# Kernel tuning notes

Hardware: AMD Instinct MI355X
Metric: run time of the kernel (lower is better)

Reference implementation:

```python
import jax, jax.numpy as jnp
import numpy as np

B, N, DIM = 4, 2048, 512
HEADS, DIM_HEAD = 8, 64
HIDDEN = HEADS * DIM_HEAD  # == DIM


def _rotary(t):
    # t: [b, h, n, d]; interleaved rotary (rotary-embedding-torch style), theta=10000
    n, d = t.shape[-2], t.shape[-1]
    inv_freq = 1.0 / (10000.0 ** (jnp.arange(0, d, 2, dtype=jnp.float32) / d))  # [d/2]
    freqs = jnp.arange(n, dtype=jnp.float32)[:, None] * inv_freq[None, :]        # [n, d/2]
    freqs = jnp.repeat(freqs, 2, axis=-1)                                        # [n, d]
    cos, sin = jnp.cos(freqs), jnp.sin(freqs)
    x1, x2 = t[..., ::2], t[..., 1::2]
    rot = jnp.stack((-x2, x1), axis=-1).reshape(t.shape)  # rotate_half, interleaved
    return t * cos + rot * sin


def setup_inputs() -> dict:
    key = jax.random.key(0)
    k1, k2, k3, k4 = jax.random.split(key, 4)
    x = jax.random.normal(k1, (B, N, DIM), dtype=jnp.float32)
    pos_bias = jax.random.normal(k2, (HEADS, N, N), dtype=jnp.float32)
    W_qkv = jax.random.normal(k3, (DIM, 3 * HIDDEN), dtype=jnp.float32) * (DIM ** -0.5)
    W_out = jax.random.normal(k4, (HIDDEN, DIM), dtype=jnp.float32) * (HIDDEN ** -0.5)
    return {"x": x, "pos_bias": pos_bias, "W_qkv": W_qkv, "W_out": W_out}


def reference(x, pos_bias, W_qkv, W_out):
    b, n, _ = x.shape
    qkv = x @ W_qkv                                   # [b, n, 3*h*d]
    q, k, v = jnp.split(qkv, 3, axis=-1)

    def to_heads(t):
        return t.reshape(b, n, HEADS, DIM_HEAD).transpose(0, 2, 1, 3)  # [b,h,n,d]

    q = to_heads(q) * (DIM_HEAD ** -0.5)
    k = to_heads(k)
    v = to_heads(v)
    q = _rotary(q)
    k = _rotary(k)
    sim = jnp.einsum('bhid,bhjd->bhij', q, k) + pos_bias[None]  # [b,h,n,n]
    attn = jax.nn.softmax(sim, axis=-1)                          # stable softmax (== amax-subtract + softmax)
    out = jnp.einsum('bhij,bhjd->bhid', attn, v)
    out = out.transpose(0, 2, 1, 3).reshape(b, n, HIDDEN)
    return out @ W_out
```

## Files before the change

kernel.cpp:

```cpp
#include <hip/hip_runtime.h>
#include <hip/hip_bf16.h>

#define DEV static __device__ __forceinline__

typedef __attribute__((ext_vector_type(8))) short s16x8;
typedef __attribute__((ext_vector_type(16))) float f32x16;

DEV float bf2f(short s) {
    unsigned u = ((unsigned)(unsigned short)s) << 16;
    union { unsigned u; float f; } c; c.u = u; return c.f;
}
DEV short f2bf(float f) {
    union { float f; unsigned u; } c; c.f = f;
    unsigned u = c.u;
    unsigned r = (u + 0x7FFFu + ((u >> 16) & 1u)) >> 16;
    return (short)r;
}

DEV f32x16 mfma(s16x8 a, s16x8 b, f32x16 c) {
    return __builtin_amdgcn_mfma_f32_32x32x16_bf16(a, b, c, 0, 0, 0);
}

__global__ void cvt_f32_bf16(const float* __restrict__ src,
                             short* __restrict__ dst, int n) {
    int i = (blockIdx.x * blockDim.x + threadIdx.x) * 4;
    if (i >= n) return;
    float4 v = *(const float4*)(src + i);
    short4 o;
    o.x = f2bf(v.x); o.y = f2bf(v.y); o.z = f2bf(v.z); o.w = f2bf(v.w);
    *(short4*)(dst + i) = o;
}

__global__ void rotab(float2* __restrict__ tab) {
    int idx = blockIdx.x * 256 + threadIdx.x;
    int n = idx >> 5, f = idx & 31;
    float inv = expf(-0.2878231366f * (float)f);
    float a = (float)n * inv;
    tab[idx] = make_float2(cosf(a), sinf(a));
}

__global__ void ktransf(const float* __restrict__ src, short* __restrict__ dst,
                        int R, int C) {
    __shared__ __align__(16) short t[32][33];
    int tx = threadIdx.x & 31, ty = threadIdx.x >> 5;
    int r0 = blockIdx.y * 32, c0 = blockIdx.x * 32;
    for (int i = 0; i < 32; i += 8)
        t[ty + i][tx] = f2bf(src[(size_t)(r0 + ty + i) * C + c0 + tx]);
    __syncthreads();
    for (int i = 0; i < 32; i += 8)
        dst[(size_t)(c0 + ty + i) * R + r0 + tx] = t[tx][ty + i];
}

__global__ __launch_bounds__(256) void gemm_qkv(
    const short* __restrict__ X, const short* __restrict__ WT,
    const float2* __restrict__ rtab,
    short* __restrict__ qws, short* __restrict__ kws, short* __restrict__ vt) {
    int wave = threadIdx.x >> 6, lane = threadIdx.x & 63;
    int l31 = lane & 31, lh = lane >> 5;
    int mw = blockIdx.x * 128 + (wave >> 1) * 64;
    int nw = blockIdx.y * 128 + (wave & 1) * 64;
    f32x16 acc[2][2] = {};
    const short* ap = X + (size_t)(mw + l31) * 512 + lh * 8;
    const short* bp = WT + (size_t)(nw + l31) * 512 + lh * 8;
#pragma unroll 4
    for (int k = 0; k < 512; k += 16) {
        s16x8 a0 = *(const s16x8*)(ap + k);
        s16x8 a1 = *(const s16x8*)(ap + 32 * 512 + k);
        s16x8 b0 = *(const s16x8*)(bp + k);
        s16x8 b1 = *(const s16x8*)(bp + 32 * 512 + k);
        acc[0][0] = mfma(a0, b0, acc[0][0]);
        acc[0][1] = mfma(a0, b1, acc[0][1]);
        acc[1][0] = mfma(a1, b0, acc[1][0]);
        acc[1][1] = mfma(a1, b1, acc[1][1]);
    }
#pragma unroll
    for (int ib = 0; ib < 2; ib++)
#pragma unroll
        for (int jb = 0; jb < 2; jb++) {
            int col = nw + jb * 32 + l31;
            int t = col >> 9;
            int cid = col & 511;
            int h = cid >> 6, d = cid & 63;
#pragma unroll
            for (int r = 0; r < 16; r++) {
                int row = (r & 3) + 8 * (r >> 2) + 4 * lh;
                int gm = mw + ib * 32 + row;
                int b = gm >> 11, n = gm & 2047;
                float v = acc[ib][jb][r];
                if (t == 0) v *= 0.125f;
                if (t < 2) {
                    float pv = __shfl_xor(v, 1);
                    float2 cs = rtab[n * 32 + (d >> 1)];
                    float o = (d & 1) ? (v * cs.x + pv * cs.y)
                                      : (v * cs.x - pv * cs.y);
                    short* dst = (t == 0) ? qws : kws;
                    dst[((size_t)(b * 8 + h) * 2048 + n) * 64 + d] = f2bf(o);
                } else {
                    vt[((size_t)(b * 8 + h) * 64 + d) * 2048 + n] = f2bf(v);
                }
            }
        }
}

#define PROW 72
__global__ __launch_bounds__(256) void attn(
    const short* __restrict__ qws, const short* __restrict__ kws,
    const short* __restrict__ vt, const float* __restrict__ bias,
    short* __restrict__ ows) {
    __shared__ __align__(16) short pls[4][32 * PROW];
    int wave = threadIdx.x >> 6, lane = threadIdx.x & 63;
    int l31 = lane & 31, lh = lane >> 5;
    int bh = blockIdx.y;
    int b = bh >> 3, h = bh & 7;
    int q0 = blockIdx.x * 128 + wave * 32;

    const short* qp = qws + ((size_t)bh * 2048 + q0 + l31) * 64 + lh * 8;
    s16x8 qf[4];
#pragma unroll
    for (int c = 0; c < 4; c++) qf[c] = *(const s16x8*)(qp + c * 16);

    f32x16 oa[2] = {};
    float lsum[16];
#pragma unroll
    for (int r = 0; r < 16; r++) lsum[r] = 0.f;
    short* pw = &pls[wave][0];
    const float* bias_base = bias + ((size_t)h * 2048 + q0) * 2048;

    for (int kt = 0; kt < 32; kt++) {
        int kb = kt * 64;
        const short* kp = kws + ((size_t)bh * 2048 + kb + l31) * 64 + lh * 8;
        f32x16 s0 = {}, s1 = {};
#pragma unroll
        for (int c = 0; c < 4; c++) {
            s16x8 k0 = *(const s16x8*)(kp + c * 16);
            s16x8 k1 = *(const s16x8*)(kp + 32 * 64 + c * 16);
            s0 = mfma(qf[c], k0, s0);
            s1 = mfma(qf[c], k1, s1);
        }
#pragma unroll
        for (int r = 0; r < 16; r++) {
            int row = (r & 3) + 8 * (r >> 2) + 4 * lh;
            const float* bp = bias_base + (size_t)row * 2048 + kb;
            float e0 = __expf(s0[r] + bp[l31]);
            float e1 = __expf(s1[r] + bp[32 + l31]);
            lsum[r] += e0 + e1;
            pw[row * PROW + l31] = f2bf(e0);
            pw[row * PROW + 32 + l31] = f2bf(e1);
        }
        const short* vp = vt + ((size_t)bh * 64 + l31) * 2048 + kb + lh * 8;
#pragma unroll
        for (int c = 0; c < 4; c++) {
            s16x8 pf = *(const s16x8*)(pw + l31 * PROW + c * 16 + lh * 8);
            s16x8 v0f = *(const s16x8*)(vp + c * 16);
            s16x8 v1f = *(const s16x8*)(vp + (size_t)32 * 2048 + c * 16);
            oa[0] = mfma(pf, v0f, oa[0]);
            oa[1] = mfma(pf, v1f, oa[1]);
        }
    }
#pragma unroll
    for (int r = 0; r < 16; r++) {
        float s = lsum[r];
#pragma unroll
        for (int off = 16; off >= 1; off >>= 1)
            s += __shfl_xor(s, off);
        float inv = 1.f / s;
        int row = (r & 3) + 8 * (r >> 2) + 4 * lh;
        size_t o0 = ((size_t)(b * 2048 + q0 + row) * 8 + h) * 64;
        ows[o0 + l31] = f2bf(oa[0][r] * inv);
        ows[o0 + 32 + l31] = f2bf(oa[1][r] * inv);
    }
}

__global__ __launch_bounds__(256) void gemm_out(
    const short* __restrict__ O, const short* __restrict__ WT,
    float* __restrict__ out) {
    int wave = threadIdx.x >> 6, lane = threadIdx.x & 63;
    int l31 = lane & 31, lh = lane >> 5;
    int m0 = blockIdx.x * 128 + (wave >> 1) * 64;
    int n0 = blockIdx.y * 128 + (wave & 1) * 64;
    f32x16 acc[2][2] = {};
    const short* ap = O + (size_t)(m0 + l31) * 512 + lh * 8;
    const short* bp = WT + (size_t)(n0 + l31) * 512 + lh * 8;
#pragma unroll 4
    for (int k = 0; k < 512; k += 16) {
        s16x8 a0 = *(const s16x8*)(ap + k);
        s16x8 a1 = *(const s16x8*)(ap + 32 * 512 + k);
        s16x8 b0 = *(const s16x8*)(bp + k);
        s16x8 b1 = *(const s16x8*)(bp + 32 * 512 + k);
        acc[0][0] = mfma(a0, b0, acc[0][0]);
        acc[0][1] = mfma(a0, b1, acc[0][1]);
        acc[1][0] = mfma(a1, b0, acc[1][0]);
        acc[1][1] = mfma(a1, b1, acc[1][1]);
    }
#pragma unroll
    for (int ib = 0; ib < 2; ib++)
#pragma unroll
        for (int jb = 0; jb < 2; jb++)
#pragma unroll
            for (int r = 0; r < 16; r++) {
                int row = (r & 3) + 8 * (r >> 2) + 4 * lh;
                out[(size_t)(m0 + ib * 32 + row) * 512 + n0 + jb * 32 + l31] =
                    acc[ib][jb][r];
            }
}

extern "C" void kernel_launch(void* const* d_in, const int* in_sizes, int n_in,
                              void* d_out, int out_size, void* d_ws,
                              size_t ws_size, hipStream_t stream) {
    const float* x    = (const float*)d_in[0];
    const float* bias = (const float*)d_in[1];
    const float* wqkv = (const float*)d_in[2];
    const float* wout = (const float*)d_in[3];
    float* out = (float*)d_out;

    char* ws = (char*)d_ws;
    short* xbf   = (short*)ws;
    short* wqkvT = xbf + 4194304;
    short* woutT = wqkvT + 786432;
    short* qws   = woutT + 262144;
    short* kws   = qws + 4194304;
    short* vt    = kws + 4194304;
    short* ows   = vt + 4194304;
    float2* rtab = (float2*)(ows + 4194304);

    cvt_f32_bf16<<<4096, 256, 0, stream>>>(x, xbf, 4194304);
    rotab<<<256, 256, 0, stream>>>(rtab);
    ktransf<<<dim3(1536 / 32, 512 / 32), 256, 0, stream>>>(wqkv, wqkvT, 512, 1536);
    ktransf<<<dim3(512 / 32, 512 / 32), 256, 0, stream>>>(wout, woutT, 512, 512);
    gemm_qkv<<<dim3(64, 12), 256, 0, stream>>>(xbf, wqkvT, rtab, qws, kws, vt);
    attn<<<dim3(16, 32), 256, 0, stream>>>(qws, kws, vt, bias, ows);
    gemm_out<<<dim3(64, 4), 256, 0, stream>>>(ows, woutT, out);
}
```

Before: 425.9 us.

## Split attention key range across two blocks and combine partial outputs

The attention kernel's 32 key tiles are now split into two halves along a new grid z dimension, doubling the number of blocks from 512 to 1024 so more of the GPU is occupied. Each half writes unnormalized fp32 partial outputs and row sums, and a new combine kernel adds the halves, normalizes and converts to bf16. Launch bounds hint at 4 blocks per CU. The workspace is re-laid out so the partial buffers alias the bf16 input and the output aliases vt. This adds extra fp32 traffic (about 32MB written and read) and one more kernel launch.

```diff
diff --git a/kernel.cpp b/kernel.cpp
--- a/kernel.cpp
+++ b/kernel.cpp
@@ -103,16 +103,17 @@
 }
 
 #define PROW 72
-__global__ __launch_bounds__(256) void attn(
+__global__ __launch_bounds__(256, 4) void attn(
     const short* __restrict__ qws, const short* __restrict__ kws,
     const short* __restrict__ vt, const float* __restrict__ bias,
-    short* __restrict__ ows) {
+    float* __restrict__ part_o, float* __restrict__ part_l) {
     __shared__ __align__(16) short pls[4][32 * PROW];
     int wave = threadIdx.x >> 6, lane = threadIdx.x & 63;
     int l31 = lane & 31, lh = lane >> 5;
     int bh = blockIdx.y;
     int b = bh >> 3, h = bh & 7;
     int q0 = blockIdx.x * 128 + wave * 32;
+    int z = blockIdx.z;
 
     const short* qp = qws + ((size_t)bh * 2048 + q0 + l31) * 64 + lh * 8;
     s16x8 qf[4];
@@ -126,7 +127,7 @@
     short* pw = &pls[wave][0];
     const float* bias_base = bias + ((size_t)h * 2048 + q0) * 2048;
 
-    for (int kt = 0; kt < 32; kt++) {
+    for (int kt = z * 16; kt < z * 16 + 16; kt++) {
         int kb = kt * 64;
         const short* kp = kws + ((size_t)bh * 2048 + kb + l31) * 64 + lh * 8;
         f32x16 s0 = {}, s1 = {};
@@ -157,18 +158,38 @@
             oa[1] = mfma(pf, v1f, oa[1]);
         }
     }
+    float* po = part_o + (size_t)z * 4194304;
 #pragma unroll
     for (int r = 0; r < 16; r++) {
         float s = lsum[r];
 #pragma unroll
         for (int off = 16; off >= 1; off >>= 1)
             s += __shfl_xor(s, off);
-        float inv = 1.f / s;
         int row = (r & 3) + 8 * (r >> 2) + 4 * lh;
         size_t o0 = ((size_t)(b * 2048 + q0 + row) * 8 + h) * 64;
-        ows[o0 + l31] = f2bf(oa[0][r] * inv);
-        ows[o0 + 32 + l31] = f2bf(oa[1][r] * inv);
-    }
+        po[o0 + l31] = oa[0][r];
+        po[o0 + 32 + l31] = oa[1][r];
+        if (l31 == 0) part_l[z * 65536 + bh * 2048 + q0 + row] = s;
+    }
+}
+
+__global__ __launch_bounds__(256) void combine(
+    const float* __restrict__ po, const float* __restrict__ pl,
+    short* __restrict__ ows) {
+    int idx = blockIdx.x * 256 + threadIdx.x;
+    int e0 = idx * 4;
+    int ro = e0 >> 6;
+    int b = ro >> 14, h = ro & 7, n = (ro >> 3) & 2047;
+    int lrow = ((b * 8 + h) << 11) + n;
+    float inv = 1.f / (pl[lrow] + pl[65536 + lrow]);
+    float4 a = *(const float4*)(po + e0);
+    float4 c = *(const float4*)(po + 4194304 + e0);
+    short4 o;
+    o.x = f2bf((a.x + c.x) * inv);
+    o.y = f2bf((a.y + c.y) * inv);
+    o.z = f2bf((a.z + c.z) * inv);
+    o.w = f2bf((a.w + c.w) * inv);
+    *(short4*)(ows + e0) = o;
 }
 
 __global__ __launch_bounds__(256) void gemm_out(
@@ -214,20 +235,23 @@
     float* out = (float*)d_out;
 
     char* ws = (char*)d_ws;
-    short* xbf   = (short*)ws;
-    short* wqkvT = xbf + 4194304;
-    short* woutT = wqkvT + 786432;
-    short* qws   = woutT + 262144;
-    short* kws   = qws + 4194304;
-    short* vt    = kws + 4194304;
-    short* ows   = vt + 4194304;
-    float2* rtab = (float2*)(ows + 4194304);
+    float* part_o = (float*)ws;
+    short* xbf    = (short*)ws;
+    float* part_l = (float*)(ws + (32u << 20));
+    short* wqkvT  = (short*)(ws + (32u << 20) + (512u << 10));
+    short* woutT  = wqkvT + 786432;
+    short* qws    = woutT + 262144;
+    short* kws    = qws + 4194304;
+    short* vt     = kws + 4194304;
+    short* ows    = vt;
+    float2* rtab  = (float2*)(vt + 4194304);
 
     cvt_f32_bf16<<<4096, 256, 0, stream>>>(x, xbf, 4194304);
     rotab<<<256, 256, 0, stream>>>(rtab);
     ktransf<<<dim3(1536 / 32, 512 / 32), 256, 0, stream>>>(wqkv, wqkvT, 512, 1536);
     ktransf<<<dim3(512 / 32, 512 / 32), 256, 0, stream>>>(wout, woutT, 512, 512);
     gemm_qkv<<<dim3(64, 12), 256, 0, stream>>>(xbf, wqkvT, rtab, qws, kws, vt);
-    attn<<<dim3(16, 32), 256, 0, stream>>>(qws, kws, vt, bias, ows);
+    attn<<<dim3(16, 32, 2), 256, 0, stream>>>(qws, kws, vt, bias, part_o, part_l);
+    combine<<<4096, 256, 0, stream>>>(part_o, part_l, ows);
     gemm_out<<<dim3(64, 4), 256, 0, stream>>>(ows, woutT, out);
 }
```

New measurement: 641.0 us. +50.5%, slower.

## Restructure attention into single-wave 16-row blocks with bias prefetch and swizzled LDS

Applied to the files above, without the earlier changes.

The attention kernel now runs one 64-thread wave per block over 16 query rows, using 16x16x32 MFMA instead of 32x32x16. Block indices are ordered so the heads that share a bias row run next to each other, and the bias tile for the next key block is prefetched into registers during the current block's compute. The P tile goes through an XOR-swizzled LDS buffer to avoid bank conflicts. The aim is to hide the latency of the large fp32 bias stream and raise occupancy, at the cost of less reuse of K and V across waves and more register pressure.

```diff
diff --git a/kernel.cpp b/kernel.cpp
--- a/kernel.cpp
+++ b/kernel.cpp
@@ -5,6 +5,7 @@
 
 typedef __attribute__((ext_vector_type(8))) short s16x8;
 typedef __attribute__((ext_vector_type(16))) float f32x16;
+typedef __attribute__((ext_vector_type(4))) float f32x4;
 
 DEV float bf2f(short s) {
     unsigned u = ((unsigned)(unsigned short)s) << 16;
@@ -19,6 +20,9 @@
 
 DEV f32x16 mfma(s16x8 a, s16x8 b, f32x16 c) {
     return __builtin_amdgcn_mfma_f32_32x32x16_bf16(a, b, c, 0, 0, 0);
+}
+DEV f32x4 mfma16(s16x8 a, s16x8 b, f32x4 c) {
+    return __builtin_amdgcn_mfma_f32_16x16x32_bf16(a, b, c, 0, 0, 0);
 }
 
 __global__ void cvt_f32_bf16(const float* __restrict__ src,
@@ -102,72 +106,102 @@
         }
 }
 
-#define PROW 72
-__global__ __launch_bounds__(256) void attn(
+__global__ __launch_bounds__(64) void attn(
     const short* __restrict__ qws, const short* __restrict__ kws,
     const short* __restrict__ vt, const float* __restrict__ bias,
     short* __restrict__ ows) {
-    __shared__ __align__(16) short pls[4][32 * PROW];
-    int wave = threadIdx.x >> 6, lane = threadIdx.x & 63;
-    int l31 = lane & 31, lh = lane >> 5;
-    int bh = blockIdx.y;
-    int b = bh >> 3, h = bh & 7;
-    int q0 = blockIdx.x * 128 + wave * 32;
-
-    const short* qp = qws + ((size_t)bh * 2048 + q0 + l31) * 64 + lh * 8;
-    s16x8 qf[4];
-#pragma unroll
-    for (int c = 0; c < 4; c++) qf[c] = *(const s16x8*)(qp + c * 16);
-
-    f32x16 oa[2] = {};
-    float lsum[16];
-#pragma unroll
-    for (int r = 0; r < 16; r++) lsum[r] = 0.f;
-    short* pw = &pls[wave][0];
-    const float* bias_base = bias + ((size_t)h * 2048 + q0) * 2048;
+    __shared__ __align__(16) short pls[16 * 64];
+    int lane = threadIdx.x;
+    int l15 = lane & 15, lh4 = lane >> 4;
+    int bid = blockIdx.x;
+    int h = bid & 7;
+    int b = (bid >> 3) & 3;
+    int q0 = (bid >> 5) * 16;
+    int bh = b * 8 + h;
+
+    const short* qp = qws + ((size_t)bh * 2048 + q0 + l15) * 64 + lh4 * 8;
+    s16x8 qf[2];
+#pragma unroll
+    for (int c = 0; c < 2; c++) qf[c] = *(const s16x8*)(qp + 32 * c);
+
+    f32x4 oa[4] = {};
+    float lsum[4] = {};
+
+    const short* kbase = kws + ((size_t)bh * 2048 + l15) * 64 + lh4 * 8;
+    const short* vbase = vt + ((size_t)bh * 64 + l15) * 2048 + lh4 * 8;
+    const float* browp = bias + ((size_t)h * 2048 + q0 + lh4 * 4) * 2048 + l15;
+
+    float bcur[16], bnxt[16];
+#pragma unroll
+    for (int j = 0; j < 4; j++)
+#pragma unroll
+        for (int r = 0; r < 4; r++)
+            bcur[j * 4 + r] = browp[(size_t)r * 2048 + 16 * j];
 
     for (int kt = 0; kt < 32; kt++) {
         int kb = kt * 64;
-        const short* kp = kws + ((size_t)bh * 2048 + kb + l31) * 64 + lh * 8;
-        f32x16 s0 = {}, s1 = {};
-#pragma unroll
-        for (int c = 0; c < 4; c++) {
-            s16x8 k0 = *(const s16x8*)(kp + c * 16);
-            s16x8 k1 = *(const s16x8*)(kp + 32 * 64 + c * 16);
-            s0 = mfma(qf[c], k0, s0);
-            s1 = mfma(qf[c], k1, s1);
-        }
-#pragma unroll
-        for (int r = 0; r < 16; r++) {
-            int row = (r & 3) + 8 * (r >> 2) + 4 * lh;
-            const float* bp = bias_base + (size_t)row * 2048 + kb;
-            float e0 = __expf(s0[r] + bp[l31]);
-            float e1 = __expf(s1[r] + bp[32 + l31]);
-            lsum[r] += e0 + e1;
-            pw[row * PROW + l31] = f2bf(e0);
-            pw[row * PROW + 32 + l31] = f2bf(e1);
-        }
-        const short* vp = vt + ((size_t)bh * 64 + l31) * 2048 + kb + lh * 8;
-#pragma unroll
-        for (int c = 0; c < 4; c++) {
-            s16x8 pf = *(const s16x8*)(pw + l31 * PROW + c * 16 + lh * 8);
-            s16x8 v0f = *(const s16x8*)(vp + c * 16);
-            s16x8 v1f = *(const s16x8*)(vp + (size_t)32 * 2048 + c * 16);
-            oa[0] = mfma(pf, v0f, oa[0]);
-            oa[1] = mfma(pf, v1f, oa[1]);
-        }
-    }
-#pragma unroll
-    for (int r = 0; r < 16; r++) {
-        float s = lsum[r];
-#pragma unroll
-        for (int off = 16; off >= 1; off >>= 1)
-            s += __shfl_xor(s, off);
-        float inv = 1.f / s;
-        int row = (r & 3) + 8 * (r >> 2) + 4 * lh;
-        size_t o0 = ((size_t)(b * 2048 + q0 + row) * 8 + h) * 64;
-        ows[o0 + l31] = f2bf(oa[0][r] * inv);
-        ows[o0 + 32 + l31] = f2bf(oa[1][r] * inv);
+        const short* kp = kbase + (size_t)kb * 64;
+        s16x8 kf[4][2];
+#pragma unroll
+        for (int j = 0; j < 4; j++)
+#pragma unroll
+            for (int c = 0; c < 2; c++)
+                kf[j][c] = *(const s16x8*)(kp + (size_t)(16 * j) * 64 + 32 * c);
+        const short* vp = vbase + kb;
+        s16x8 vf[2][4];
+#pragma unroll
+        for (int m = 0; m < 2; m++)
+#pragma unroll
+            for (int j2 = 0; j2 < 4; j2++)
+                vf[m][j2] = *(const s16x8*)(vp + (size_t)(16 * j2) * 2048 + 32 * m);
+        f32x4 s[4] = {};
+#pragma unroll
+        for (int j = 0; j < 4; j++) {
+            s[j] = mfma16(qf[0], kf[j][0], s[j]);
+            s[j] = mfma16(qf[1], kf[j][1], s[j]);
+        }
+        if (kt < 31) {
+            const float* bnp = browp + (size_t)(kb + 64);
+#pragma unroll
+            for (int j = 0; j < 4; j++)
+#pragma unroll
+                for (int r = 0; r < 4; r++)
+                    bnxt[j * 4 + r] = bnp[(size_t)r * 2048 + 16 * j];
+        }
+        __builtin_amdgcn_sched_barrier(0);
+#pragma unroll
+        for (int j = 0; j < 4; j++)
+#pragma unroll
+            for (int r = 0; r < 4; r++) {
+                float e = __expf(s[j][r] + bcur[j * 4 + r]);
+                lsum[r] += e;
+                int q = lh4 * 4 + r;
+                pls[q * 64 + ((16 * j + l15) ^ ((q & 7) << 3))] = f2bf(e);
+            }
+        s16x8 pa[2];
+#pragma unroll
+        for (int m = 0; m < 2; m++)
+            pa[m] = *(const s16x8*)(
+                pls + l15 * 64 + ((32 * m + lh4 * 8) ^ ((l15 & 7) << 3)));
+#pragma unroll
+        for (int j2 = 0; j2 < 4; j2++) {
+            oa[j2] = mfma16(pa[0], vf[0][j2], oa[j2]);
+            oa[j2] = mfma16(pa[1], vf[1][j2], oa[j2]);
+        }
+#pragma unroll
+        for (int i = 0; i < 16; i++) bcur[i] = bnxt[i];
+    }
+#pragma unroll
+    for (int r = 0; r < 4; r++) {
+#pragma unroll
+        for (int off = 8; off >= 1; off >>= 1)
+            lsum[r] += __shfl_xor(lsum[r], off);
+        float inv = 1.f / lsum[r];
+        int q = lh4 * 4 + r;
+        size_t o0 = ((size_t)(b * 2048 + q0 + q) * 8 + h) * 64;
+#pragma unroll
+        for (int j2 = 0; j2 < 4; j2++)
+            ows[o0 + 16 * j2 + l15] = f2bf(oa[j2][r] * inv);
     }
 }
 
@@ -228,6 +262,6 @@
     ktransf<<<dim3(1536 / 32, 512 / 32), 256, 0, stream>>>(wqkv, wqkvT, 512, 1536);
     ktransf<<<dim3(512 / 32, 512 / 32), 256, 0, stream>>>(wout, woutT, 512, 512);
     gemm_qkv<<<dim3(64, 12), 256, 0, stream>>>(xbf, wqkvT, rtab, qws, kws, vt);
-    attn<<<dim3(16, 32), 256, 0, stream>>>(qws, kws, vt, bias, ows);
+    attn<<<4096, 64, 0, stream>>>(qws, kws, vt, bias, ows);
     gemm_out<<<dim3(64, 4), 256, 0, stream>>>(ows, woutT, out);
 }
```

Result: slower. 518.8 us (+21.8%).
